# Kernel optimization log

Hardware: AMD Instinct MI355X
Metric: run time of the kernel (lower is better)

Reference implementation:

```python
import jax, jax.numpy as jnp
import numpy as np

EMBED = 4
H1, H2 = 8, 4


def setup_inputs() -> dict:
    key = jax.random.key(0)
    ks = jax.random.split(key, 10)
    x = jax.random.normal(ks[0], (1024, 256, EMBED), dtype=jnp.float32)
    Wq = jax.random.normal(ks[1], (EMBED, EMBED), dtype=jnp.float32)
    Wk = jax.random.normal(ks[2], (EMBED, EMBED), dtype=jnp.float32)
    Wv = jax.random.normal(ks[3], (EMBED, EMBED), dtype=jnp.float32)
    # nn.Linear default init: U(-1/sqrt(fan_in), 1/sqrt(fan_in)); approximate with uniform
    def lin(k, fan_in, fan_out):
        k1, k2 = jax.random.split(k)
        bound = 1.0 / np.sqrt(fan_in)
        W = jax.random.uniform(k1, (fan_in, fan_out), minval=-bound, maxval=bound, dtype=jnp.float32)
        b = jax.random.uniform(k2, (fan_out,), minval=-bound, maxval=bound, dtype=jnp.float32)
        return W, b
    W1, b1 = lin(ks[4], EMBED, H1)
    W2, b2 = lin(ks[5], H1, H2)
    W3, b3 = lin(ks[6], H2, 1)
    return {"x": x, "Wq": Wq, "Wk": Wk, "Wv": Wv,
            "W1": W1, "b1": b1, "W2": W2, "b2": b2, "W3": W3, "b3": b3}


def reference(x, Wq, Wk, Wv, W1, b1, W2, b2, W3, b3):
    # Self-attention: x [B, S, E]
    q = x @ Wq
    k = x @ Wk
    v = x @ Wv
    scale = 1.0 / np.sqrt(EMBED).astype(np.float32)
    scores = jax.nn.softmax(jnp.einsum('bse,bte->bst', q, k) * scale, axis=-1)
    attn_out = jnp.einsum('bst,bte->bse', scores, v)
    h = jnp.tanh(attn_out @ W1 + b1)
    h = jnp.tanh(h @ W2 + b2)
    return h @ W3 + b3  # [B, S, 1]
```

## Files before the change

kernel.cpp:

```cpp
#include <hip/hip_runtime.h>
#include <math.h>

constexpr int S  = 256;
constexpr int E  = 4;
constexpr int H1 = 8;
constexpr int H2 = 4;

typedef __attribute__((ext_vector_type(8))) _Float16 half8;
typedef __attribute__((ext_vector_type(8))) short    bf16x8;
typedef __attribute__((ext_vector_type(4))) float    f32x4;
typedef __attribute__((ext_vector_type(4))) int      i32x4;

__device__ __forceinline__ float fast_tanh(float x) {
    const float z = __builtin_amdgcn_exp2f(x * 2.88539008f);
    return 1.f - 2.f * __builtin_amdgcn_rcpf(z + 1.f);
}

__device__ __forceinline__ void split16(float x, unsigned short& hi, unsigned short& lo) {
    _Float16 h = (_Float16)x;
    float r = x - (float)h;
    _Float16 l = (_Float16)r;
    hi = __builtin_bit_cast(unsigned short, h);
    lo = __builtin_bit_cast(unsigned short, l);
}

__device__ __forceinline__ unsigned short bf16_rne(float x) {
    unsigned u = __builtin_bit_cast(unsigned, x);
    u = (u + 0x7FFFu + ((u >> 16) & 1u)) >> 16;
    return (unsigned short)u;
}
__device__ __forceinline__ float bf16_as_f32(unsigned short h) {
    return __builtin_bit_cast(float, (unsigned)h << 16);
}

__device__ __forceinline__ unsigned pk_bf16(float a, float b) {
    return __builtin_amdgcn_perm(__builtin_bit_cast(unsigned, b),
                                 __builtin_bit_cast(unsigned, a), 0x07060302u);
}
__device__ __forceinline__ float hi_part(float a) {
    return __builtin_bit_cast(float, __builtin_bit_cast(unsigned, a) & 0xFFFF0000u);
}

__device__ __forceinline__ half8 frag(int a, int b, int c, int d) {
    i32x4 t = {a, b, c, d};
    return __builtin_bit_cast(half8, t);
}
__device__ __forceinline__ bf16x8 bfrag(int a, int b, int c, int d) {
    i32x4 t = {a, b, c, d};
    return __builtin_bit_cast(bf16x8, t);
}
__device__ __forceinline__ f32x4 mfma_f16(half8 a, half8 b, f32x4 c) {
    return __builtin_amdgcn_mfma_f32_16x16x32_f16(a, b, c, 0, 0, 0);
}
__device__ __forceinline__ f32x4 mfma_bf16(bf16x8 a, bf16x8 b, f32x4 c) {
    return __builtin_amdgcn_mfma_f32_16x16x32_bf16(a, b, c, 0, 0, 0);
}

__global__ __launch_bounds__(256, 4) void attn_mlp_kernel(
    const float* __restrict__ x,
    const float* __restrict__ Wq, const float* __restrict__ Wk, const float* __restrict__ Wv,
    const float* __restrict__ W1, const float* __restrict__ b1,
    const float* __restrict__ W2, const float* __restrict__ b2,
    const float* __restrict__ W3, const float* __restrict__ b3,
    float* __restrict__ out)
{
    const int b    = blockIdx.x;
    const int tid  = threadIdx.x;
    const int w    = tid >> 6;
    const int lane = tid & 63;
    const int g    = lane >> 4;
    const int c15  = lane & 15;

    __shared__ i32x4 qrec[S];
    __shared__ i32x4 krec[S];
    __shared__ __align__(16) unsigned short vhT[16][264];
    __shared__ __align__(16) unsigned short vlT[16][264];
    __shared__ float mh_lds[S];
    __shared__ float accb[S][9];
    __shared__ float kmax_lds[4];

    const float4 xr = *reinterpret_cast<const float4*>(x + ((size_t)b * S + tid) * E);
    const float xv[E] = {xr.x, xr.y, xr.z, xr.w};
    float qq = 0.f, kk = 0.f;
    {
        float q[E], k[E], v[E];
        #pragma unroll
        for (int e = 0; e < E; ++e) {
            float aq = 0.f, ak = 0.f, av = 0.f;
            #pragma unroll
            for (int i = 0; i < E; ++i) {
                aq = fmaf(xv[i], Wq[i * E + e], aq);
                ak = fmaf(xv[i], Wk[i * E + e], ak);
                av = fmaf(xv[i], Wv[i * E + e], av);
            }
            q[e] = aq * 0.72134752f;
            k[e] = ak;
            v[e] = av;
            qq = fmaf(q[e], q[e], qq);
            kk = fmaf(ak, ak, kk);
        }
        unsigned short qh[4], ql[4], kh[4], kl[4];
        #pragma unroll
        for (int e = 0; e < E; ++e) {
            split16(q[e], qh[e], ql[e]);
            split16(k[e], kh[e], kl[e]);
        }
        qrec[tid] = (i32x4){ (int)(qh[0] | (qh[1] << 16)), (int)(qh[2] | (qh[3] << 16)),
                             (int)(ql[0] | (ql[1] << 16)), (int)(ql[2] | (ql[3] << 16)) };
        krec[tid] = (i32x4){ (int)(kh[0] | (kh[1] << 16)), (int)(kh[2] | (kh[3] << 16)),
                             (int)(kl[0] | (kl[1] << 16)), (int)(kl[2] | (kl[3] << 16)) };
        #pragma unroll
        for (int e = 0; e < E; ++e) {
            const unsigned short vh = bf16_rne(v[e]);
            const unsigned short vl = bf16_rne(v[e] - bf16_as_f32(vh));
            vhT[e][tid] = vh;
            vlT[e][tid] = vl;
        }
        vhT[4][tid] = 0x3F80;
        #pragma unroll
        for (int r = 5; r < 16; ++r) vhT[r][tid] = 0;
        #pragma unroll
        for (int r = 4; r < 16; ++r) vlT[r][tid] = 0;

        #pragma unroll
        for (int off = 32; off > 0; off >>= 1)
            kk = fmaxf(kk, __shfl_xor(kk, off));
        if (lane == 0) kmax_lds[w] = kk;
    }
    __syncthreads();
    const float kmax2 = fmaxf(fmaxf(kmax_lds[0], kmax_lds[1]),
                              fmaxf(kmax_lds[2], kmax_lds[3]));
    mh_lds[tid] = -sqrtf(qq * kmax2);
    __syncthreads();

    half8 Bq[4];
    float negmh[4];
    f32x4 acc[4];
    #pragma unroll
    for (int rt = 0; rt < 4; ++rt) {
        const int s = 64 * w + 16 * rt + c15;
        i32x4 u = qrec[s];
        int h0 = (g == 0) ? u[0] : u[2];
        int h1 = (g == 0) ? u[1] : u[3];
        if (g >= 2) { h0 = 0; h1 = 0; }
        Bq[rt] = frag(h0, h1, h0, h1);
        negmh[rt] = mh_lds[s];
        acc[rt] = (f32x4){0.f, 0.f, 0.f, 0.f};
    }

    #pragma unroll 1
    for (int ch = 0; ch < 8; ++ch) {
        const int kb = ch * 32;
        i32x4 k0 = krec[kb + c15];
        i32x4 k1 = krec[kb + 16 + c15];
        if (g >= 2) { k0 = (i32x4){0,0,0,0}; k1 = (i32x4){0,0,0,0}; }
        const half8 Ak0 = __builtin_bit_cast(half8, k0);
        const half8 Ak1 = __builtin_bit_cast(half8, k1);

        const int vi = kb + 4 * g;
        const uint2 h0 = *(const uint2*)&vhT[c15][vi];
        const uint2 h1 = *(const uint2*)&vhT[c15][vi + 16];
        const uint2 l0 = *(const uint2*)&vlT[c15][vi];
        const uint2 l1 = *(const uint2*)&vlT[c15][vi + 16];
        const bf16x8 Bvh0 = bfrag((int)h0.x, (int)h0.y, (int)h0.x, (int)h0.y);
        const bf16x8 Bvh1 = bfrag((int)h1.x, (int)h1.y, (int)h1.x, (int)h1.y);
        const bf16x8 Bvl  = bfrag((int)l0.x, (int)l0.y, (int)l1.x, (int)l1.y);

        #pragma unroll
        for (int rt = 0; rt < 4; ++rt) {
            const f32x4 cm = {negmh[rt], negmh[rt], negmh[rt], negmh[rt]};
            const f32x4 c0 = mfma_f16(Ak0, Bq[rt], cm);
            const f32x4 c1 = mfma_f16(Ak1, Bq[rt], cm);
            const float p0 = __builtin_amdgcn_exp2f(c0[0]);
            const float p1 = __builtin_amdgcn_exp2f(c0[1]);
            const float p2 = __builtin_amdgcn_exp2f(c0[2]);
            const float p3 = __builtin_amdgcn_exp2f(c0[3]);
            const float p4 = __builtin_amdgcn_exp2f(c1[0]);
            const float p5 = __builtin_amdgcn_exp2f(c1[1]);
            const float p6 = __builtin_amdgcn_exp2f(c1[2]);
            const float p7 = __builtin_amdgcn_exp2f(c1[3]);
            const unsigned hi01 = pk_bf16(p0, p1), hi23 = pk_bf16(p2, p3);
            const unsigned hi45 = pk_bf16(p4, p5), hi67 = pk_bf16(p6, p7);
            const unsigned lo01 = pk_bf16(p0 - hi_part(p0), p1 - hi_part(p1));
            const unsigned lo23 = pk_bf16(p2 - hi_part(p2), p3 - hi_part(p3));
            const unsigned lo45 = pk_bf16(p4 - hi_part(p4), p5 - hi_part(p5));
            const unsigned lo67 = pk_bf16(p6 - hi_part(p6), p7 - hi_part(p7));
            const bf16x8 A10 = bfrag((int)hi01, (int)hi23, (int)lo01, (int)lo23);
            const bf16x8 A11 = bfrag((int)hi45, (int)hi67, (int)lo45, (int)lo67);
            const bf16x8 A2  = bfrag((int)hi01, (int)hi23, (int)hi45, (int)hi67);
            acc[rt] = mfma_bf16(A10, Bvh0, acc[rt]);
            acc[rt] = mfma_bf16(A11, Bvh1, acc[rt]);
            acc[rt] = mfma_bf16(A2,  Bvl,  acc[rt]);
        }
    }

    #pragma unroll
    for (int rt = 0; rt < 4; ++rt) {
        if (c15 < 5) {
            const int row = 64 * w + 16 * rt + 4 * g;
            #pragma unroll
            for (int i = 0; i < 4; ++i) accb[row + i][c15] = acc[rt][i];
        }
    }
    __syncthreads();

    const float inv = 1.0f / fmaxf(accb[tid][4], 1e-37f);
    float a[E];
    #pragma unroll
    for (int e = 0; e < E; ++e) a[e] = accb[tid][e] * inv;

    float h1v[H1];
    #pragma unroll
    for (int o = 0; o < H1; ++o) {
        float s = b1[o];
        #pragma unroll
        for (int i = 0; i < E; ++i) s = fmaf(a[i], W1[i * H1 + o], s);
        h1v[o] = fast_tanh(s);
    }
    float h2v[H2];
    #pragma unroll
    for (int o = 0; o < H2; ++o) {
        float s = b2[o];
        #pragma unroll
        for (int i = 0; i < H1; ++i) s = fmaf(h1v[i], W2[i * H2 + o], s);
        h2v[o] = fast_tanh(s);
    }
    float r = b3[0];
    #pragma unroll
    for (int i = 0; i < H2; ++i) r = fmaf(h2v[i], W3[i], r);

    out[(size_t)b * S + tid] = r;
}

extern "C" void kernel_launch(void* const* d_in, const int* in_sizes, int n_in,
                              void* d_out, int out_size, void* d_ws, size_t ws_size,
                              hipStream_t stream) {
    const float* x  = (const float*)d_in[0];
    const float* Wq = (const float*)d_in[1];
    const float* Wk = (const float*)d_in[2];
    const float* Wv = (const float*)d_in[3];
    const float* W1 = (const float*)d_in[4];
    const float* b1 = (const float*)d_in[5];
    const float* W2 = (const float*)d_in[6];
    const float* b2 = (const float*)d_in[7];
    const float* W3 = (const float*)d_in[8];
    const float* b3 = (const float*)d_in[9];
    float* out = (float*)d_out;

    const int B = in_sizes[0] / (S * E);
    attn_mlp_kernel<<<dim3(B), dim3(256), 0, stream>>>(
        x, Wq, Wk, Wv, W1, b1, W2, b2, W3, b3, out);
}
```

Baseline: 88.82 us.

## Split each batch's queries across two blocks and compact V LDS layout

Launches two blocks per batch, each handling 128 query rows, so each wave processes 2 row tiles instead of 4. Both blocks still recompute the Q/K/V projections for all 256 tokens. The separate padded V-hi/V-lo LDS arrays become one 8-row buffer, and the ones row and zero padding are synthesized in registers with selects. This shrinks LDS per block, and the launch-bounds occupancy hint is raised from 4 to 5. The aim is more blocks and waves in flight and better latency hiding, at the cost of duplicated projection work and half the threads idling in the MLP epilogue.

```diff
diff --git a/kernel.cpp b/kernel.cpp
--- a/kernel.cpp
+++ b/kernel.cpp
@@ -56,7 +56,7 @@
     return __builtin_amdgcn_mfma_f32_16x16x32_bf16(a, b, c, 0, 0, 0);
 }
 
-__global__ __launch_bounds__(256, 4) void attn_mlp_kernel(
+__global__ __launch_bounds__(256, 5) void attn_mlp_kernel(
     const float* __restrict__ x,
     const float* __restrict__ Wq, const float* __restrict__ Wk, const float* __restrict__ Wv,
     const float* __restrict__ W1, const float* __restrict__ b1,
@@ -64,7 +64,9 @@
     const float* __restrict__ W3, const float* __restrict__ b3,
     float* __restrict__ out)
 {
-    const int b    = blockIdx.x;
+    const int blk   = blockIdx.x;
+    const int b     = blk >> 1;
+    const int qbase = (blk & 1) << 7;
     const int tid  = threadIdx.x;
     const int w    = tid >> 6;
     const int lane = tid & 63;
@@ -73,10 +75,9 @@
 
     __shared__ i32x4 qrec[S];
     __shared__ i32x4 krec[S];
-    __shared__ __align__(16) unsigned short vhT[16][264];
-    __shared__ __align__(16) unsigned short vlT[16][264];
+    __shared__ __align__(16) unsigned short vcomb[8][264];
     __shared__ float mh_lds[S];
-    __shared__ float accb[S][9];
+    __shared__ float accb[128][5];
     __shared__ float kmax_lds[4];
 
     const float4 xr = *reinterpret_cast<const float4*>(x + ((size_t)b * S + tid) * E);
@@ -113,15 +114,9 @@
         for (int e = 0; e < E; ++e) {
             const unsigned short vh = bf16_rne(v[e]);
             const unsigned short vl = bf16_rne(v[e] - bf16_as_f32(vh));
-            vhT[e][tid] = vh;
-            vlT[e][tid] = vl;
-        }
-        vhT[4][tid] = 0x3F80;
-        #pragma unroll
-        for (int r = 5; r < 16; ++r) vhT[r][tid] = 0;
-        #pragma unroll
-        for (int r = 4; r < 16; ++r) vlT[r][tid] = 0;
-
+            vcomb[e][tid]     = vh;
+            vcomb[4 + e][tid] = vl;
+        }
         #pragma unroll
         for (int off = 32; off > 0; off >>= 1)
             kk = fmaxf(kk, __shfl_xor(kk, off));
@@ -133,12 +128,12 @@
     mh_lds[tid] = -sqrtf(qq * kmax2);
     __syncthreads();
 
-    half8 Bq[4];
-    float negmh[4];
-    f32x4 acc[4];
+    half8 Bq[2];
+    float negmh[2];
+    f32x4 acc[2];
     #pragma unroll
-    for (int rt = 0; rt < 4; ++rt) {
-        const int s = 64 * w + 16 * rt + c15;
+    for (int rt = 0; rt < 2; ++rt) {
+        const int s = qbase + 32 * w + 16 * rt + c15;
         i32x4 u = qrec[s];
         int h0 = (g == 0) ? u[0] : u[2];
         int h1 = (g == 0) ? u[1] : u[3];
@@ -147,6 +142,12 @@
         negmh[rt] = mh_lds[s];
         acc[rt] = (f32x4){0.f, 0.f, 0.f, 0.f};
     }
+
+    const bool is4 = (c15 == 4);
+    const bool lt4 = (c15 < 4);
+    const unsigned ONES2 = 0x3F803F80u;
+    const int vrh = (c15 & 7);
+    const int vrl = 4 + (c15 & 3);
 
     #pragma unroll 1
     for (int ch = 0; ch < 8; ++ch) {
@@ -158,16 +159,20 @@
         const half8 Ak1 = __builtin_bit_cast(half8, k1);
 
         const int vi = kb + 4 * g;
-        const uint2 h0 = *(const uint2*)&vhT[c15][vi];
-        const uint2 h1 = *(const uint2*)&vhT[c15][vi + 16];
-        const uint2 l0 = *(const uint2*)&vlT[c15][vi];
-        const uint2 l1 = *(const uint2*)&vlT[c15][vi + 16];
-        const bf16x8 Bvh0 = bfrag((int)h0.x, (int)h0.y, (int)h0.x, (int)h0.y);
-        const bf16x8 Bvh1 = bfrag((int)h1.x, (int)h1.y, (int)h1.x, (int)h1.y);
-        const bf16x8 Bvl  = bfrag((int)l0.x, (int)l0.y, (int)l1.x, (int)l1.y);
-
-        #pragma unroll
-        for (int rt = 0; rt < 4; ++rt) {
+        const uint2 h0 = *(const uint2*)&vcomb[vrh][vi];
+        const uint2 h1 = *(const uint2*)&vcomb[vrh][vi + 16];
+        const uint2 l0 = *(const uint2*)&vcomb[vrl][vi];
+        const uint2 l1 = *(const uint2*)&vcomb[vrl][vi + 16];
+        const unsigned hx0 = is4 ? ONES2 : h0.x, hy0 = is4 ? ONES2 : h0.y;
+        const unsigned hx1 = is4 ? ONES2 : h1.x, hy1 = is4 ? ONES2 : h1.y;
+        const unsigned lx0 = lt4 ? l0.x : 0u,    ly0 = lt4 ? l0.y : 0u;
+        const unsigned lx1 = lt4 ? l1.x : 0u,    ly1 = lt4 ? l1.y : 0u;
+        const bf16x8 Bvh0 = bfrag((int)hx0, (int)hy0, (int)hx0, (int)hy0);
+        const bf16x8 Bvh1 = bfrag((int)hx1, (int)hy1, (int)hx1, (int)hy1);
+        const bf16x8 Bvl  = bfrag((int)lx0, (int)ly0, (int)lx1, (int)ly1);
+
+        #pragma unroll
+        for (int rt = 0; rt < 2; ++rt) {
             const f32x4 cm = {negmh[rt], negmh[rt], negmh[rt], negmh[rt]};
             const f32x4 c0 = mfma_f16(Ak0, Bq[rt], cm);
             const f32x4 c1 = mfma_f16(Ak1, Bq[rt], cm);
@@ -195,41 +200,43 @@
     }
 
     #pragma unroll
-    for (int rt = 0; rt < 4; ++rt) {
+    for (int rt = 0; rt < 2; ++rt) {
         if (c15 < 5) {
-            const int row = 64 * w + 16 * rt + 4 * g;
+            const int row = 32 * w + 16 * rt + 4 * g;
             #pragma unroll
             for (int i = 0; i < 4; ++i) accb[row + i][c15] = acc[rt][i];
         }
     }
     __syncthreads();
 
-    const float inv = 1.0f / fmaxf(accb[tid][4], 1e-37f);
-    float a[E];
-    #pragma unroll
-    for (int e = 0; e < E; ++e) a[e] = accb[tid][e] * inv;
-
-    float h1v[H1];
-    #pragma unroll
-    for (int o = 0; o < H1; ++o) {
-        float s = b1[o];
-        #pragma unroll
-        for (int i = 0; i < E; ++i) s = fmaf(a[i], W1[i * H1 + o], s);
-        h1v[o] = fast_tanh(s);
-    }
-    float h2v[H2];
-    #pragma unroll
-    for (int o = 0; o < H2; ++o) {
-        float s = b2[o];
-        #pragma unroll
-        for (int i = 0; i < H1; ++i) s = fmaf(h1v[i], W2[i * H2 + o], s);
-        h2v[o] = fast_tanh(s);
-    }
-    float r = b3[0];
-    #pragma unroll
-    for (int i = 0; i < H2; ++i) r = fmaf(h2v[i], W3[i], r);
-
-    out[(size_t)b * S + tid] = r;
+    if (tid < 128) {
+        const float inv = 1.0f / fmaxf(accb[tid][4], 1e-37f);
+        float a[E];
+        #pragma unroll
+        for (int e = 0; e < E; ++e) a[e] = accb[tid][e] * inv;
+
+        float h1v[H1];
+        #pragma unroll
+        for (int o = 0; o < H1; ++o) {
+            float s = b1[o];
+            #pragma unroll
+            for (int i = 0; i < E; ++i) s = fmaf(a[i], W1[i * H1 + o], s);
+            h1v[o] = fast_tanh(s);
+        }
+        float h2v[H2];
+        #pragma unroll
+        for (int o = 0; o < H2; ++o) {
+            float s = b2[o];
+            #pragma unroll
+            for (int i = 0; i < H1; ++i) s = fmaf(h1v[i], W2[i * H2 + o], s);
+            h2v[o] = fast_tanh(s);
+        }
+        float r = b3[0];
+        #pragma unroll
+        for (int i = 0; i < H2; ++i) r = fmaf(h2v[i], W3[i], r);
+
+        out[(size_t)b * S + qbase + tid] = r;
+    }
 }
 
 extern "C" void kernel_launch(void* const* d_in, const int* in_sizes, int n_in,
@@ -248,6 +255,6 @@
     float* out = (float*)d_out;
 
     const int B = in_sizes[0] / (S * E);
-    attn_mlp_kernel<<<dim3(B), dim3(256), 0, stream>>>(
+    attn_mlp_kernel<<<dim3(B * 2), dim3(256), 0, stream>>>(
         x, Wq, Wk, Wv, W1, b1, W2, b2, W3, b3, out);
 }
```

After: 90.99 us. +2.4%, slower.
